# Kernel tuning notes

Measured on AMD Instinct MI355X. Metric: run time of the kernel, lower is better.

Reference implementation:

```python
import jax, jax.numpy as jnp
import numpy as np

CHUNK = 16
GROUPS = 8
EPS = 1e-5


def setup_inputs() -> dict:
    key = jax.random.key(0)
    ks = jax.random.split(key, 8)
    B, C, H, W = 8, 1, 2048, 2048
    D_in = C * CHUNK * CHUNK  # 256
    D = 16                    # out_channels
    x = jax.random.normal(ks[0], (B, C, H, W), dtype=jnp.float32)
    s_fc = 1.0 / np.sqrt(D_in)
    fc_wr = jax.random.normal(ks[1], (D, D_in), dtype=jnp.float32) * s_fc
    fc_wi = jax.random.normal(ks[2], (D, D_in), dtype=jnp.float32) * s_fc
    fc_br = jax.random.normal(ks[3], (D,), dtype=jnp.float32) * s_fc
    fc_bi = jax.random.normal(ks[4], (D,), dtype=jnp.float32) * s_fc
    conv_w = jax.random.normal(ks[5], (D, D), dtype=jnp.float32) * (1.0 / np.sqrt(D))
    conv_b = jax.random.normal(ks[6], (D,), dtype=jnp.float32) * 0.05
    gamma = jnp.ones((D,), dtype=jnp.float32)
    beta = jnp.zeros((D,), dtype=jnp.float32)
    return {"x": x, "fc_wr": fc_wr, "fc_wi": fc_wi, "fc_br": fc_br,
            "fc_bi": fc_bi, "conv_w": conv_w, "conv_b": conv_b,
            "gamma": gamma, "beta": beta}


def reference(x, fc_wr, fc_wi, fc_br, fc_bi, conv_w, conv_b, gamma, beta):
    B, C, H, W = x.shape
    s = CHUNK
    h, w = H // s, W // s
    D = fc_wr.shape[0]
    # rearrange 'b c (h s1) (w s2) -> (b h w) (s1 s2 c)'
    p = x.reshape(B, C, h, s, w, s)
    p = p.transpose(0, 2, 4, 3, 5, 1).reshape(B * h * w, s * s * C)
    # FFT over the flattened patch dim (ortho norm) -> complex64
    fft = jnp.fft.fft(p, norm="ortho")
    Wc = fc_wr + 1j * fc_wi           # [D, D_in] complex
    bc = fc_br + 1j * fc_bi           # [D]
    fc = fft @ Wc.T + bc              # [N, D] complex linear
    # IFFT over channel dim (size D), keep real part
    y = jnp.fft.ifft(fc, norm="ortho").real  # [N, D] float32
    # '(b h w) d -> b d h w'
    y = y.reshape(B, h, w, D).transpose(0, 3, 1, 2)
    # 1x1 conv
    y = jnp.einsum("bdhw,ed->behw", y, conv_w) + conv_b[None, :, None, None]
    # GroupNorm(GROUPS, D)
    yg = y.reshape(B, GROUPS, D // GROUPS, h, w)
    mean = yg.mean(axis=(2, 3, 4), keepdims=True)
    var = yg.var(axis=(2, 3, 4), keepdims=True)
    yn = ((yg - mean) * jax.lax.rsqrt(var + EPS)).reshape(B, D, h, w)
    return yn * gamma[None, :, None, None] + beta[None, :, None, None]
```

## Files before the change

kernel.cpp:

```cpp
#include <hip/hip_runtime.h>
#include <math.h>

#define PI_F 3.14159265358979323846f


#define WS_M     0
#define WS_V     4096
#define WS_A     4352
#define WS_U     8448
#define WS_STATS 8464

__global__ void prep1(const float* __restrict__ wr, const float* __restrict__ wi,
                      const float* __restrict__ br, const float* __restrict__ bi,
                      float* __restrict__ M, float* __restrict__ v) {
    const int m = blockIdx.x;
    const int t = threadIdx.x;
    __shared__ float Tr[256], Ti[256], cosT[256], sinT[256], cd[16], sd[16];

    float ang = (2.0f * PI_F / 256.0f) * (float)t;
    cosT[t] = cosf(ang);
    sinT[t] = sinf(ang);
    if (t < 16) {
        float a = (2.0f * PI_F / 16.0f) * (float)((t * m) & 15);
        cd[t] = cosf(a);
        sd[t] = sinf(a);
    }
    __syncthreads();

    float tr = 0.f, ti = 0.f;
    #pragma unroll
    for (int d = 0; d < 16; ++d) {
        float wrv = wr[d * 256 + t];
        float wiv = wi[d * 256 + t];
        tr += wrv * cd[d] - wiv * sd[d];
        ti += wrv * sd[d] + wiv * cd[d];
    }
    Tr[t] = tr;
    Ti[t] = ti;
    __syncthreads();

    float acc = 0.f;
    for (int k = 0; k < 256; ++k) {
        int a = (k * t) & 255;
        acc += Tr[k] * cosT[a] + Ti[k] * sinT[a];
    }
    M[m * 256 + t] = acc * (1.0f / 64.0f);

    if (t == 0) {
        float s = 0.f;
        #pragma unroll
        for (int d = 0; d < 16; ++d) {
            float a = (2.0f * PI_F / 16.0f) * (float)((d * m) & 15);
            s += br[d] * cosf(a) - bi[d] * sinf(a);
        }
        v[m] = 0.25f * s;
    }
}

__global__ void prep2(const float* __restrict__ conv_w, const float* __restrict__ conv_b,
                      const float* __restrict__ M, const float* __restrict__ v,
                      float* __restrict__ A, float* __restrict__ u,
                      float* __restrict__ stats) {
    const int t = threadIdx.x;
    __shared__ float cw[256];
    __shared__ float Ms[16][256];
    cw[t] = conv_w[t];
    #pragma unroll
    for (int m = 0; m < 16; ++m) Ms[m][t] = M[m * 256 + t];
    __syncthreads();

    #pragma unroll
    for (int e = 0; e < 16; ++e) {
        float acc = 0.f;
        #pragma unroll
        for (int m = 0; m < 16; ++m) acc += cw[e * 16 + m] * Ms[m][t];
        A[e * 256 + t] = acc;
    }
    if (t < 16) {
        float acc = conv_b[t];
        #pragma unroll
        for (int m = 0; m < 16; ++m) acc += cw[t * 16 + m] * v[m];
        u[t] = acc;
    }
    if (t < 128) stats[t] = 0.f;
}

__global__ __launch_bounds__(256) void main_k(const float* __restrict__ x,
                                              const float* __restrict__ ws,
                                              float* __restrict__ out,
                                              float* __restrict__ stats) {
    __shared__ float As[4096];
    __shared__ float Us[16];
    __shared__ float s_sum[8], s_ssq[8];
    const int t = threadIdx.x;

    const float4* Ag  = (const float4*)(ws + WS_A);
    float4*       As4 = (float4*)As;
    #pragma unroll
    for (int i = 0; i < 4; ++i) As4[t + 256 * i] = Ag[t + 256 * i];
    if (t < 16) Us[t] = ws[WS_U + t];
    if (t < 8) { s_sum[t] = 0.f; s_ssq[t] = 0.f; }
    __syncthreads();

    const int P  = (blockIdx.x << 8) + t;
    const int b  = P >> 14;
    const int pi = P & 16383;
    const int ph = pi >> 7;
    const int pw = pi & 127;

    const float* xb = x + ((size_t)b << 22) + (size_t)(ph * 16) * 2048 + (size_t)(pw * 16);

    float acc[16];
    #pragma unroll
    for (int e = 0; e < 16; ++e) acc[e] = 0.f;

    for (int s1 = 0; s1 < 16; ++s1) {
        const float4* rp = (const float4*)(xb + (size_t)s1 * 2048);
        float4 p0 = rp[0], p1 = rp[1], p2 = rp[2], p3 = rp[3];
        const int nb = s1 << 4;
        #pragma unroll
        for (int e = 0; e < 16; ++e) {
            const float* Ae = As + (e << 8) + nb;
            const float4 a0 = *(const float4*)(Ae + 0);
            const float4 a1 = *(const float4*)(Ae + 4);
            const float4 a2 = *(const float4*)(Ae + 8);
            const float4 a3 = *(const float4*)(Ae + 12);
            acc[e] += a0.x * p0.x + a0.y * p0.y + a0.z * p0.z + a0.w * p0.w
                    + a1.x * p1.x + a1.y * p1.y + a1.z * p1.z + a1.w * p1.w
                    + a2.x * p2.x + a2.y * p2.y + a2.z * p2.z + a2.w * p2.w
                    + a3.x * p3.x + a3.y * p3.y + a3.z * p3.z + a3.w * p3.w;
        }
    }

    float sv[8], qv[8];
    const size_t obase = ((size_t)b << 18) + (size_t)(ph << 7) + (size_t)pw;
    #pragma unroll
    for (int g = 0; g < 8; ++g) {
        float v0 = acc[2 * g]     + Us[2 * g];
        float v1 = acc[2 * g + 1] + Us[2 * g + 1];
        out[obase + (size_t)(2 * g) * 16384]     = v0;
        out[obase + (size_t)(2 * g + 1) * 16384] = v1;
        sv[g] = v0 + v1;
        qv[g] = v0 * v0 + v1 * v1;
    }
    #pragma unroll
    for (int off = 32; off > 0; off >>= 1) {
        #pragma unroll
        for (int g = 0; g < 8; ++g) {
            sv[g] += __shfl_xor(sv[g], off, 64);
            qv[g] += __shfl_xor(qv[g], off, 64);
        }
    }
    if ((t & 63) == 0) {
        #pragma unroll
        for (int g = 0; g < 8; ++g) {
            atomicAdd(&s_sum[g], sv[g]);
            atomicAdd(&s_ssq[g], qv[g]);
        }
    }
    __syncthreads();
    if (t < 8) {
        atomicAdd(&stats[b * 8 + t],      s_sum[t]);
        atomicAdd(&stats[64 + b * 8 + t], s_ssq[t]);
    }
}

__global__ __launch_bounds__(256) void finalize(float* __restrict__ out,
                                                const float* __restrict__ stats,
                                                const float* __restrict__ gamma,
                                                const float* __restrict__ beta) {
    const int i    = blockIdx.x * 256 + threadIdx.x;
    const int flat = i << 2;
    const int b = flat >> 18;
    const int c = (flat >> 14) & 15;
    const int g = c >> 1;

    const float inv_n = 1.0f / 32768.0f;
    float mean = stats[b * 8 + g] * inv_n;
    float var  = stats[64 + b * 8 + g] * inv_n - mean * mean;
    float rstd = rsqrtf(var + 1e-5f);
    float sc = rstd * gamma[c];
    float sh = beta[c] - mean * sc;

    float4 vv = ((float4*)out)[i];
    vv.x = vv.x * sc + sh;
    vv.y = vv.y * sc + sh;
    vv.z = vv.z * sc + sh;
    vv.w = vv.w * sc + sh;
    ((float4*)out)[i] = vv;
}

extern "C" void kernel_launch(void* const* d_in, const int* in_sizes, int n_in,
                              void* d_out, int out_size, void* d_ws, size_t ws_size,
                              hipStream_t stream) {
    const float* x  = (const float*)d_in[0];
    const float* wr = (const float*)d_in[1];
    const float* wi = (const float*)d_in[2];
    const float* br = (const float*)d_in[3];
    const float* bi = (const float*)d_in[4];
    const float* cw = (const float*)d_in[5];
    const float* cb = (const float*)d_in[6];
    const float* gm = (const float*)d_in[7];
    const float* bt = (const float*)d_in[8];
    float* out = (float*)d_out;
    float* ws  = (float*)d_ws;

    prep1<<<16, 256, 0, stream>>>(wr, wi, br, bi, ws + WS_M, ws + WS_V);
    prep2<<<1, 256, 0, stream>>>(cw, cb, ws + WS_M, ws + WS_V,
                                 ws + WS_A, ws + WS_U, ws + WS_STATS);
    main_k<<<512, 256, 0, stream>>>(x, ws, out, ws + WS_STATS);
    finalize<<<2048, 256, 0, stream>>>(out, ws + WS_STATS, gm, bt);
}
```

Before: 226.8 us.

## Register-block four patches per lane and split rows across lanes with shuffle reduction

Reorganizes the main kernel so each lane loads four consecutive rows spanning four adjacent patches, and reuses each A-matrix fragment loaded from LDS across all four patches. Partial sums over row groups are then combined with cross-lane shuffles, and each lane writes one patch. The A tile in LDS is padded (row stride 20, block stride 320) so that lanes reading different rows avoid bank conflicts. The aim is to cut LDS load traffic per FMA and widen the per-lane global loads. The cost is far more registers per lane (64 accumulators plus 64 loaded values), which lowers occupancy, and an added shuffle reduction over 64 values.

```diff
diff --git a/kernel.cpp b/kernel.cpp
--- a/kernel.cpp
+++ b/kernel.cpp
@@ -85,59 +85,98 @@
     if (t < 128) stats[t] = 0.f;
 }
 
-__global__ __launch_bounds__(256) void main_k(const float* __restrict__ x,
-                                              const float* __restrict__ ws,
-                                              float* __restrict__ out,
-                                              float* __restrict__ stats) {
-    __shared__ float As[4096];
+__global__ __launch_bounds__(256, 2) void main_k(const float* __restrict__ x,
+                                                 const float* __restrict__ ws,
+                                                 float* __restrict__ out,
+                                                 float* __restrict__ stats) {
+    __shared__ float As[16 * 320];
     __shared__ float Us[16];
     __shared__ float s_sum[8], s_ssq[8];
     const int t = threadIdx.x;
 
-    const float4* Ag  = (const float4*)(ws + WS_A);
-    float4*       As4 = (float4*)As;
-    #pragma unroll
-    for (int i = 0; i < 4; ++i) As4[t + 256 * i] = Ag[t + 256 * i];
+    {
+        const int e = t >> 4, s1 = t & 15;
+        const float4* src = (const float4*)(ws + WS_A + e * 256 + s1 * 16);
+        float* dst = As + e * 320 + s1 * 20;
+        float4 v0 = src[0], v1 = src[1], v2 = src[2], v3 = src[3];
+        *(float4*)(dst + 0)  = v0;
+        *(float4*)(dst + 4)  = v1;
+        *(float4*)(dst + 8)  = v2;
+        *(float4*)(dst + 12) = v3;
+    }
     if (t < 16) Us[t] = ws[WS_U + t];
     if (t < 8) { s_sum[t] = 0.f; s_ssq[t] = 0.f; }
     __syncthreads();
 
-    const int P  = (blockIdx.x << 8) + t;
-    const int b  = P >> 14;
-    const int pi = P & 16383;
+    const int wv   = t >> 6;
+    const int lane = t & 63;
+    const int j    = lane & 15;
+    const int pg   = lane >> 4;
+
+    const int Pbase = (blockIdx.x << 8) + (wv << 6) + (j << 2);
+    const int b  = Pbase >> 14;
+    const int pi = Pbase & 16383;
     const int ph = pi >> 7;
     const int pw = pi & 127;
 
-    const float* xb = x + ((size_t)b << 22) + (size_t)(ph * 16) * 2048 + (size_t)(pw * 16);
-
-    float acc[16];
-    #pragma unroll
-    for (int e = 0; e < 16; ++e) acc[e] = 0.f;
-
-    for (int s1 = 0; s1 < 16; ++s1) {
-        const float4* rp = (const float4*)(xb + (size_t)s1 * 2048);
-        float4 p0 = rp[0], p1 = rp[1], p2 = rp[2], p3 = rp[3];
-        const int nb = s1 << 4;
+    const float* xb = x + ((size_t)b << 22)
+                        + (size_t)(ph * 16 + pg * 4) * 2048
+                        + (size_t)(pw * 16);
+
+    float acc[4][16];
+    #pragma unroll
+    for (int p = 0; p < 4; ++p)
+        #pragma unroll
+        for (int e = 0; e < 16; ++e) acc[p][e] = 0.f;
+
+    #pragma unroll
+    for (int r = 0; r < 4; ++r) {
+        const float4* rp = (const float4*)(xb + (size_t)r * 2048);
+        float4 pr[16];
+        #pragma unroll
+        for (int i = 0; i < 16; ++i) pr[i] = rp[i];
+
+        const int s1 = (pg << 2) + r;
+        const float* Arow = As + s1 * 20;
         #pragma unroll
         for (int e = 0; e < 16; ++e) {
-            const float* Ae = As + (e << 8) + nb;
+            const float* Ae = Arow + e * 320;
             const float4 a0 = *(const float4*)(Ae + 0);
             const float4 a1 = *(const float4*)(Ae + 4);
             const float4 a2 = *(const float4*)(Ae + 8);
             const float4 a3 = *(const float4*)(Ae + 12);
-            acc[e] += a0.x * p0.x + a0.y * p0.y + a0.z * p0.z + a0.w * p0.w
-                    + a1.x * p1.x + a1.y * p1.y + a1.z * p1.z + a1.w * p1.w
-                    + a2.x * p2.x + a2.y * p2.y + a2.z * p2.z + a2.w * p2.w
-                    + a3.x * p3.x + a3.y * p3.y + a3.z * p3.z + a3.w * p3.w;
-        }
-    }
+            #pragma unroll
+            for (int p = 0; p < 4; ++p) {
+                const float4 q0 = pr[p * 4 + 0];
+                const float4 q1 = pr[p * 4 + 1];
+                const float4 q2 = pr[p * 4 + 2];
+                const float4 q3 = pr[p * 4 + 3];
+                acc[p][e] += a0.x * q0.x + a0.y * q0.y + a0.z * q0.z + a0.w * q0.w
+                           + a1.x * q1.x + a1.y * q1.y + a1.z * q1.z + a1.w * q1.w
+                           + a2.x * q2.x + a2.y * q2.y + a2.z * q2.z + a2.w * q2.w
+                           + a3.x * q3.x + a3.y * q3.y + a3.z * q3.z + a3.w * q3.w;
+            }
+        }
+    }
+
+    #pragma unroll
+    for (int p = 0; p < 4; ++p)
+        #pragma unroll
+        for (int e = 0; e < 16; ++e)
+            acc[p][e] += __shfl_xor(acc[p][e], 16, 64);
+    #pragma unroll
+    for (int p = 0; p < 4; ++p)
+        #pragma unroll
+        for (int e = 0; e < 16; ++e)
+            acc[p][e] += __shfl_xor(acc[p][e], 32, 64);
+
+    const size_t obase = ((size_t)b << 18) + (size_t)(ph << 7) + (size_t)(pw + pg);
 
     float sv[8], qv[8];
-    const size_t obase = ((size_t)b << 18) + (size_t)(ph << 7) + (size_t)pw;
     #pragma unroll
     for (int g = 0; g < 8; ++g) {
-        float v0 = acc[2 * g]     + Us[2 * g];
-        float v1 = acc[2 * g + 1] + Us[2 * g + 1];
+        float v0 = acc[pg][2 * g]     + Us[2 * g];
+        float v1 = acc[pg][2 * g + 1] + Us[2 * g + 1];
         out[obase + (size_t)(2 * g) * 16384]     = v0;
         out[obase + (size_t)(2 * g + 1) * 16384] = v1;
         sv[g] = v0 + v1;
```

New measurement: 360.6 us. +59.0%, slower.

## Compute patch projection with fp16 MFMA and coalesced LDS-staged output

Applied to the files above, without the earlier changes.

Rewrites the main projection kernel to use MFMA 16x16x32 f16 instructions. The precomputed fused matrix is stored as fp16 in workspace, and input patches are converted to fp16 on the fly. Each block now handles 64 patches (2048 blocks) and stages results through LDS so the output writes become coalesced float4 stores, which also simplifies the group-stat reduction. This removes the heavy scalar FMA work, but fp16 rounding of both inputs and weights reduces accuracy, and the input read pattern changes.

```diff
diff --git a/kernel.cpp b/kernel.cpp
--- a/kernel.cpp
+++ b/kernel.cpp
@@ -9,6 +9,10 @@
 #define WS_A     4352
 #define WS_U     8448
 #define WS_STATS 8464
+#define WS_AH    8592
+
+using half8  = __attribute__((ext_vector_type(8))) _Float16;
+using floatx4 = __attribute__((ext_vector_type(4))) float;
 
 __global__ void prep1(const float* __restrict__ wr, const float* __restrict__ wi,
                       const float* __restrict__ br, const float* __restrict__ bi,
@@ -59,9 +63,10 @@
 
 __global__ void prep2(const float* __restrict__ conv_w, const float* __restrict__ conv_b,
                       const float* __restrict__ M, const float* __restrict__ v,
-                      float* __restrict__ A, float* __restrict__ u,
-                      float* __restrict__ stats) {
+                      float* __restrict__ ws) {
     const int t = threadIdx.x;
+    float* A = ws + WS_A;
+    _Float16* Ah = (_Float16*)(ws + WS_AH);
     __shared__ float cw[256];
     __shared__ float Ms[16][256];
     cw[t] = conv_w[t];
@@ -75,88 +80,98 @@
         #pragma unroll
         for (int m = 0; m < 16; ++m) acc += cw[e * 16 + m] * Ms[m][t];
         A[e * 256 + t] = acc;
+        Ah[e * 256 + t] = (_Float16)acc;
     }
     if (t < 16) {
         float acc = conv_b[t];
         #pragma unroll
         for (int m = 0; m < 16; ++m) acc += cw[t * 16 + m] * v[m];
-        u[t] = acc;
-    }
-    if (t < 128) stats[t] = 0.f;
+        ws[WS_U + t] = acc;
+    }
+    if (t < 128) ws[WS_STATS + t] = 0.f;
 }
 
 __global__ __launch_bounds__(256) void main_k(const float* __restrict__ x,
                                               const float* __restrict__ ws,
                                               float* __restrict__ out,
                                               float* __restrict__ stats) {
-    __shared__ float As[4096];
+    __shared__ _Float16 A_sh[16 * 264];
+    __shared__ float out_s[64 * 17];
     __shared__ float Us[16];
     __shared__ float s_sum[8], s_ssq[8];
     const int t = threadIdx.x;
 
-    const float4* Ag  = (const float4*)(ws + WS_A);
-    float4*       As4 = (float4*)As;
-    #pragma unroll
-    for (int i = 0; i < 4; ++i) As4[t + 256 * i] = Ag[t + 256 * i];
+    {
+        const uint4* asrc = (const uint4*)(ws + WS_AH);
+        uint4 q0 = asrc[t * 2];
+        uint4 q1 = asrc[t * 2 + 1];
+        _Float16* dp = A_sh + (t >> 4) * 264 + (t & 15) * 16;
+        *(uint4*)dp       = q0;
+        *(uint4*)(dp + 8) = q1;
+    }
     if (t < 16) Us[t] = ws[WS_U + t];
     if (t < 8) { s_sum[t] = 0.f; s_ssq[t] = 0.f; }
     __syncthreads();
 
-    const int P  = (blockIdx.x << 8) + t;
-    const int b  = P >> 14;
-    const int pi = P & 16383;
-    const int ph = pi >> 7;
-    const int pw = pi & 127;
-
-    const float* xb = x + ((size_t)b << 22) + (size_t)(ph * 16) * 2048 + (size_t)(pw * 16);
-
-    float acc[16];
-    #pragma unroll
-    for (int e = 0; e < 16; ++e) acc[e] = 0.f;
-
-    for (int s1 = 0; s1 < 16; ++s1) {
-        const float4* rp = (const float4*)(xb + (size_t)s1 * 2048);
-        float4 p0 = rp[0], p1 = rp[1], p2 = rp[2], p3 = rp[3];
-        const int nb = s1 << 4;
-        #pragma unroll
-        for (int e = 0; e < 16; ++e) {
-            const float* Ae = As + (e << 8) + nb;
-            const float4 a0 = *(const float4*)(Ae + 0);
-            const float4 a1 = *(const float4*)(Ae + 4);
-            const float4 a2 = *(const float4*)(Ae + 8);
-            const float4 a3 = *(const float4*)(Ae + 12);
-            acc[e] += a0.x * p0.x + a0.y * p0.y + a0.z * p0.z + a0.w * p0.w
-                    + a1.x * p1.x + a1.y * p1.y + a1.z * p1.z + a1.w * p1.w
-                    + a2.x * p2.x + a2.y * p2.y + a2.z * p2.z + a2.w * p2.w
-                    + a3.x * p3.x + a3.y * p3.y + a3.z * p3.z + a3.w * p3.w;
-        }
-    }
-
-    float sv[8], qv[8];
-    const size_t obase = ((size_t)b << 18) + (size_t)(ph << 7) + (size_t)pw;
-    #pragma unroll
-    for (int g = 0; g < 8; ++g) {
-        float v0 = acc[2 * g]     + Us[2 * g];
-        float v1 = acc[2 * g + 1] + Us[2 * g + 1];
-        out[obase + (size_t)(2 * g) * 16384]     = v0;
-        out[obase + (size_t)(2 * g + 1) * 16384] = v1;
-        sv[g] = v0 + v1;
-        qv[g] = v0 * v0 + v1 * v1;
-    }
-    #pragma unroll
-    for (int off = 32; off > 0; off >>= 1) {
-        #pragma unroll
-        for (int g = 0; g < 8; ++g) {
-            sv[g] += __shfl_xor(sv[g], off, 64);
-            qv[g] += __shfl_xor(qv[g], off, 64);
-        }
-    }
-    if ((t & 63) == 0) {
-        #pragma unroll
-        for (int g = 0; g < 8; ++g) {
-            atomicAdd(&s_sum[g], sv[g]);
-            atomicAdd(&s_ssq[g], qv[g]);
-        }
+    const int w    = t >> 6;
+    const int lane = t & 63;
+    const int m    = lane & 15;
+    const int kg   = lane >> 4;
+
+    const int P0  = blockIdx.x << 6;
+    const int b   = P0 >> 14;
+    const int pi  = P0 & 16383;
+    const int ph  = pi >> 7;
+    const int pw0 = pi & 127;
+
+    const float* xb = x + ((size_t)b << 22)
+                        + (size_t)(ph << 4) * 2048
+                        + (size_t)((pw0 + w * 16 + m) << 4);
+
+    floatx4 acc = {0.f, 0.f, 0.f, 0.f};
+    const int r_off = (kg >> 1);
+    const int c_off = (kg & 1) << 3;
+
+    #pragma unroll
+    for (int s = 0; s < 8; ++s) {
+        const float* px = xb + (size_t)(2 * s + r_off) * 2048 + c_off;
+        float4 x0 = *(const float4*)px;
+        float4 x1 = *(const float4*)(px + 4);
+        half8 a;
+        a[0] = (_Float16)x0.x; a[1] = (_Float16)x0.y;
+        a[2] = (_Float16)x0.z; a[3] = (_Float16)x0.w;
+        a[4] = (_Float16)x1.x; a[5] = (_Float16)x1.y;
+        a[6] = (_Float16)x1.z; a[7] = (_Float16)x1.w;
+        half8 bf = *(const half8*)&A_sh[m * 264 + s * 32 + kg * 8];
+        acc = __builtin_amdgcn_mfma_f32_16x16x32_f16(a, bf, acc, 0, 0, 0);
+    }
+
+    #pragma unroll
+    for (int r = 0; r < 4; ++r)
+        out_s[(w * 16 + kg * 4 + r) * 17 + m] = acc[r];
+    __syncthreads();
+
+    const int ch = t >> 4;
+    const int i4 = t & 15;
+    const float u = Us[ch];
+    float v0 = out_s[(i4 * 4 + 0) * 17 + ch] + u;
+    float v1 = out_s[(i4 * 4 + 1) * 17 + ch] + u;
+    float v2 = out_s[(i4 * 4 + 2) * 17 + ch] + u;
+    float v3 = out_s[(i4 * 4 + 3) * 17 + ch] + u;
+    *(float4*)&out[((size_t)b << 18) + (size_t)ch * 16384
+                   + (size_t)(ph << 7) + (size_t)(pw0 + i4 * 4)]
+        = make_float4(v0, v1, v2, v3);
+
+    float sv = v0 + v1 + v2 + v3;
+    float qv = v0 * v0 + v1 * v1 + v2 * v2 + v3 * v3;
+    #pragma unroll
+    for (int off = 1; off <= 16; off <<= 1) {
+        sv += __shfl_xor(sv, off, 64);
+        qv += __shfl_xor(qv, off, 64);
+    }
+    if ((lane & 31) == 0) {
+        atomicAdd(&s_sum[ch >> 1], sv);
+        atomicAdd(&s_ssq[ch >> 1], qv);
     }
     __syncthreads();
     if (t < 8) {
@@ -206,8 +221,7 @@
     float* ws  = (float*)d_ws;
 
     prep1<<<16, 256, 0, stream>>>(wr, wi, br, bi, ws + WS_M, ws + WS_V);
-    prep2<<<1, 256, 0, stream>>>(cw, cb, ws + WS_M, ws + WS_V,
-                                 ws + WS_A, ws + WS_U, ws + WS_STATS);
-    main_k<<<512, 256, 0, stream>>>(x, ws, out, ws + WS_STATS);
+    prep2<<<1, 256, 0, stream>>>(cw, cb, ws + WS_M, ws + WS_V, ws);
+    main_k<<<2048, 256, 0, stream>>>(x, ws, out, ws + WS_STATS);
     finalize<<<2048, 256, 0, stream>>>(out, ws + WS_STATS, gm, bt);
 }
```

Measured after the change: 224.3 us. No clear change (-1.1%).
